# Kernel tuning notes

Hardware: AMD Instinct MI355X
Metric: run time of the kernel (lower is better)

Reference implementation:

```python
import jax, jax.numpy as jnp
import numpy as np

V, E, H, L = 512, 128, 256, 4
B, T = 128, 1024


def setup_inputs() -> dict:
    key = jax.random.key(0)
    ks = jax.random.split(key, 16)
    s = 0.05
    inp = {
        "x": jax.random.randint(ks[0], (B, T), 0, V),
        "tags": jax.random.randint(ks[1], (B, T), 0, L),
        "mask": jnp.ones((B, T), dtype=bool),
        "emb": jax.random.normal(ks[2], (V, E), jnp.float32) * s,
        "w_ih_f": jax.random.normal(ks[3], (3 * H, E), jnp.float32) * s,
        "w_hh_f": jax.random.normal(ks[4], (3 * H, H), jnp.float32) * s,
        "b_ih_f": jax.random.normal(ks[5], (3 * H,), jnp.float32) * s,
        "b_hh_f": jax.random.normal(ks[6], (3 * H,), jnp.float32) * s,
        "w_ih_b": jax.random.normal(ks[7], (3 * H, E), jnp.float32) * s,
        "w_hh_b": jax.random.normal(ks[8], (3 * H, H), jnp.float32) * s,
        "b_ih_b": jax.random.normal(ks[9], (3 * H,), jnp.float32) * s,
        "b_hh_b": jax.random.normal(ks[10], (3 * H,), jnp.float32) * s,
        "fc_w": jax.random.normal(ks[11], (L, 2 * H), jnp.float32) * s,
        "fc_b": jax.random.normal(ks[12], (L,), jnp.float32) * s,
        "start_trans": jax.random.normal(ks[13], (L,), jnp.float32) * 0.1,
        "end_trans": jax.random.normal(ks[14], (L,), jnp.float32) * 0.1,
        "trans": jax.random.normal(ks[15], (L, L), jnp.float32) * 0.1,
    }
    return inp


def _gru_scan(xe, w_ih, w_hh, b_ih, b_hh):
    # xe: [B,T,E] -> out [B,T,H]; PyTorch GRU gate order: r, z, n
    gi = jnp.einsum("bte,ge->btg", xe, w_ih) + b_ih  # [B,T,3H]
    gi = jnp.swapaxes(gi, 0, 1)  # [T,B,3H]
    h0 = jnp.zeros((xe.shape[0], H), xe.dtype)

    def step(h, gi_t):
        gh = h @ w_hh.T + b_hh
        i_r, i_z, i_n = jnp.split(gi_t, 3, axis=-1)
        h_r, h_z, h_n = jnp.split(gh, 3, axis=-1)
        r = jax.nn.sigmoid(i_r + h_r)
        z = jax.nn.sigmoid(i_z + h_z)
        n = jnp.tanh(i_n + r * h_n)
        h_new = (1.0 - z) * n + z * h
        return h_new, h_new

    _, out = jax.lax.scan(step, h0, gi)
    return jnp.swapaxes(out, 0, 1)  # [B,T,H]


def _crf_neg_llh(emissions, tags, mask, start_trans, end_trans, trans):
    # emissions [B,T,L], tags [B,T] int, mask [B,T] bool
    maskf = mask.astype(emissions.dtype)
    # ----- numerator: score of gold path -----
    em_sel = jnp.take_along_axis(emissions, tags[..., None], axis=2)[..., 0]  # [B,T]
    trans_sel = trans[tags[:, :-1], tags[:, 1:]]  # [B,T-1]
    score = start_trans[tags[:, 0]] + em_sel[:, 0]
    score = score + jnp.sum((trans_sel + em_sel[:, 1:]) * maskf[:, 1:], axis=1)
    seq_ends = jnp.sum(mask.astype(jnp.int32), axis=1) - 1  # [B]
    last_tags = jnp.take_along_axis(tags, seq_ends[:, None], axis=1)[:, 0]
    score = score + end_trans[last_tags]
    # ----- denominator: forward algorithm (logsumexp scan) -----
    alpha0 = start_trans[None, :] + emissions[:, 0]  # [B,L]
    em_rest = jnp.swapaxes(emissions[:, 1:], 0, 1)  # [T-1,B,L]
    m_rest = jnp.swapaxes(mask[:, 1:], 0, 1)  # [T-1,B]

    def step(alpha, inputs):
        emit_t, m_t = inputs
        nxt = jax.nn.logsumexp(alpha[:, :, None] + trans[None] + emit_t[:, None, :], axis=1)
        alpha = jnp.where(m_t[:, None], nxt, alpha)
        return alpha, None

    alpha, _ = jax.lax.scan(step, alpha0, (em_rest, m_rest))
    logZ = jax.nn.logsumexp(alpha + end_trans[None, :], axis=1)  # [B]
    llh = score - logZ
    return -jnp.mean(llh)  # reduction='mean', negated in Segmenter.forward


def reference(x, tags, mask, emb, w_ih_f, w_hh_f, b_ih_f, b_hh_f,
              w_ih_b, w_hh_b, b_ih_b, b_hh_b, fc_w, fc_b,
              start_trans, end_trans, trans):
    xe = emb[x]  # [B,T,E]
    out_f = _gru_scan(xe, w_ih_f, w_hh_f, b_ih_f, b_hh_f)
    out_b = _gru_scan(xe[:, ::-1], w_ih_b, w_hh_b, b_ih_b, b_hh_b)[:, ::-1]
    gru_out = jnp.concatenate([out_f, out_b], axis=-1)  # [B,T,2H]
    emissions = jnp.einsum("bth,lh->btl", gru_out, fc_w) + fc_b  # [B,T,L]
    return _crf_neg_llh(emissions, tags, mask, start_trans, end_trans, trans)
```

## Files before the change

### kernel.cpp

```cpp
#include <hip/hip_runtime.h>
#include <hip/hip_fp16.h>

#define Tn 1024
#define NB 128

#define S_RZ (-1.4426950408889634f)
#define S_N  (-2.8853900817779268f)

typedef _Float16 h2_t  __attribute__((ext_vector_type(2)));
typedef _Float16 f16x8 __attribute__((ext_vector_type(8)));
typedef float    f32x4 __attribute__((ext_vector_type(4)));

__device__ __forceinline__ float dot2f(h2_t a, h2_t b, float c) {
#if __has_builtin(__builtin_amdgcn_fdot2)
  return __builtin_amdgcn_fdot2(a, b, c, false);
#else
  return c + (float)a[0] * (float)b[0] + (float)a[1] * (float)b[1];
#endif
}

__device__ __forceinline__ h2_t u2h(unsigned u) {
  union { unsigned u; h2_t h; } c; c.u = u; return c.h;
}

template <int CTRL>
__device__ __forceinline__ float dppadd(float v) {
  int i = __builtin_bit_cast(int, v);
  int r = __builtin_amdgcn_update_dpp(i, i, CTRL, 0xF, 0xF, true);
  return v + __builtin_bit_cast(float, r);
}

__global__ __launch_bounds__(768)
void gv_build(const float* __restrict__ emb,
              const float* __restrict__ wihf, const float* __restrict__ bihf, const float* __restrict__ bhhf,
              const float* __restrict__ wihb, const float* __restrict__ bihb, const float* __restrict__ bhhb,
              float* __restrict__ gvp)
{
  const int d  = blockIdx.x >> 7;
  const int v4 = (blockIdx.x & 127) * 4;
  const float* wih = d ? wihb : wihf;
  const float* bih = d ? bihb : bihf;
  const float* bhh = d ? bhhb : bhhf;
  __shared__ float se[4][128];
  const int tid = threadIdx.x;
  if (tid < 512) se[tid >> 7][tid & 127] = emb[(v4 + (tid >> 7)) * 128 + (tid & 127)];
  __syncthreads();
  const int row = tid;
  const float b0 = bih[row];
  float a0 = b0, a1 = b0, a2 = b0, a3 = b0;
  #pragma unroll
  for (int e = 0; e < 128; e += 4) {
    const float4 w = *reinterpret_cast<const float4*>(&wih[row * 128 + e]);
    a0 = fmaf(w.x, se[0][e], a0); a0 = fmaf(w.y, se[0][e+1], a0);
    a0 = fmaf(w.z, se[0][e+2], a0); a0 = fmaf(w.w, se[0][e+3], a0);
    a1 = fmaf(w.x, se[1][e], a1); a1 = fmaf(w.y, se[1][e+1], a1);
    a1 = fmaf(w.z, se[1][e+2], a1); a1 = fmaf(w.w, se[1][e+3], a1);
    a2 = fmaf(w.x, se[2][e], a2); a2 = fmaf(w.y, se[2][e+1], a2);
    a2 = fmaf(w.z, se[2][e+2], a2); a2 = fmaf(w.w, se[2][e+3], a2);
    a3 = fmaf(w.x, se[3][e], a3); a3 = fmaf(w.y, se[3][e+1], a3);
    a3 = fmaf(w.z, se[3][e+2], a3); a3 = fmaf(w.w, se[3][e+3], a3);
  }
  const int g  = row >> 8, j = row & 255;
  const int w  = j >> 5, tu = (j >> 4) & 1, c = j & 15;
  const float sc  = (g == 2) ? S_N : S_RZ;
  const float add = (g < 2) ? bhh[row] : 0.f;
  const int slot = ((w * 2 + tu) * 3 + g) * 16 + c;
  float* out = gvp + (size_t)(d * 512 + v4) * 768 + slot;
  out[0]    = sc * (a0 + add);
  out[768]  = sc * (a1 + add);
  out[1536] = sc * (a2 + add);
  out[2304] = sc * (a3 + add);
}

__global__ __launch_bounds__(512, 2)
void gru_scan(const int* __restrict__ x,
              const float* __restrict__ gvp,
              const float* __restrict__ whhf,
              const float* __restrict__ whhb,
              const float* __restrict__ bhhf,
              const float* __restrict__ bhhb,
              const float* __restrict__ fcw,
              float* __restrict__ em)
{
  const int tid = threadIdx.x;
  const int w   = tid >> 6;
  const int l   = tid & 63;
  const int c   = l & 15;
  const int lg  = l >> 4;
  const int dir = blockIdx.x & 1;
  const int b   = blockIdx.x >> 1;

  const float* whh = dir ? whhb : whhf;
  const float* bhh = dir ? bhhb : bhhf;

  __shared__ __align__(16) _Float16 hls[2][256];
  __shared__ float gvs[2][768];
  __shared__ float els[2][8];

  if (tid < 64) reinterpret_cast<uint4*>(hls)[tid] = make_uint4(0, 0, 0, 0);

  f16x8 bf[3][2][8];
  #pragma unroll
  for (int g = 0; g < 3; ++g) {
    const float sc = (g == 2) ? S_N : S_RZ;
    #pragma unroll
    for (int tu = 0; tu < 2; ++tu) {
      const float* wrow = whh + (size_t)(g * 256 + w * 32 + tu * 16 + c) * 256 + lg * 8;
      #pragma unroll
      for (int ks = 0; ks < 8; ++ks) {
        const float4 f0 = *reinterpret_cast<const float4*>(wrow + ks * 32);
        const float4 f1 = *reinterpret_cast<const float4*>(wrow + ks * 32 + 4);
        f16x8 v;
        v[0] = (_Float16)(f0.x * sc); v[1] = (_Float16)(f0.y * sc);
        v[2] = (_Float16)(f0.z * sc); v[3] = (_Float16)(f0.w * sc);
        v[4] = (_Float16)(f1.x * sc); v[5] = (_Float16)(f1.y * sc);
        v[6] = (_Float16)(f1.z * sc); v[7] = (_Float16)(f1.w * sc);
        bf[g][tu][ks] = v;
      }
    }
  }

  const float bn0 = S_N * bhh[512 + w * 32 + c];
  const float bn1 = S_N * bhh[512 + w * 32 + 16 + c];

  const int lab = tid >> 7;
  const int kp  = tid & 127;
  h2_t fce;
  fce[0] = (_Float16)fcw[lab * 512 + dir * 256 + 2 * kp];
  fce[1] = (_Float16)fcw[lab * 512 + dir * 256 + 2 * kp + 1];

  const int*   xb  = x + b * Tn;
  float*       emo = em + (size_t)(dir * NB + b) * (Tn * 4);
  const float* gvd = gvp + (size_t)dir * (512 * 768);

  {
    const float* gr = gvd + (size_t)xb[dir ? (Tn - 1) : 0] * 768;
    gvs[0][tid] = gr[tid];
    if (tid < 256) gvs[0][tid + 512] = gr[tid + 512];
  }
  float ho0 = 0.f, ho1 = 0.f;
  __syncthreads();

  for (int t = 0; t < Tn; ++t) {
    const int cur = t & 1;

    const int tn1 = (t + 1 < Tn) ? (t + 1) : (Tn - 1);
    const float* gr = gvd + (size_t)xb[dir ? (Tn - 1 - tn1) : tn1] * 768;
    const float su0 = gr[tid];
    const float su1 = (tid < 256) ? gr[tid + 512] : 0.f;

    {
      const unsigned hq = *reinterpret_cast<const unsigned*>(&hls[cur][kp * 2]);
      float pa = dot2f(fce, u2h(hq), 0.f);
      pa = dppadd<0xB1>(pa);
      pa = dppadd<0x4E>(pa);
      pa = dppadd<0x141>(pa);
      pa = dppadd<0x140>(pa);
      pa += __shfl_xor(pa, 16);
      pa += __shfl_xor(pa, 32);
      if (l == 0) els[cur][w] = pa;
    }
    if (t >= 2 && tid < 4) {
      const float v = els[cur ^ 1][2 * tid] + els[cur ^ 1][2 * tid + 1];
      const int ptt = dir ? (Tn + 1 - t) : (t - 2);
      emo[ptt * 4 + tid] = v;
    }

    const float* gc = gvs[cur] + w * 96 + c;
    f32x4 aR0 = {gc[0],  0.f, 0.f, 0.f};
    f32x4 aZ0 = {gc[16], 0.f, 0.f, 0.f};
    f32x4 aN0 = {bn0,    0.f, 0.f, 0.f};
    f32x4 aR1 = {gc[48], 0.f, 0.f, 0.f};
    f32x4 aZ1 = {gc[64], 0.f, 0.f, 0.f};
    f32x4 aN1 = {bn1,    0.f, 0.f, 0.f};
    const float gin0 = gc[32];
    const float gin1 = gc[80];

    const _Float16* hc = hls[cur];
    #pragma unroll
    for (int ks = 0; ks < 4; ++ks) {
      const f16x8 a = *reinterpret_cast<const f16x8*>(hc + ks * 32 + lg * 8);
      aR0 = __builtin_amdgcn_mfma_f32_16x16x32_f16(a, bf[0][0][ks], aR0, 0, 0, 0);
      aZ0 = __builtin_amdgcn_mfma_f32_16x16x32_f16(a, bf[1][0][ks], aZ0, 0, 0, 0);
      aN0 = __builtin_amdgcn_mfma_f32_16x16x32_f16(a, bf[2][0][ks], aN0, 0, 0, 0);
      aR1 = __builtin_amdgcn_mfma_f32_16x16x32_f16(a, bf[0][1][ks], aR1, 0, 0, 0);
      aZ1 = __builtin_amdgcn_mfma_f32_16x16x32_f16(a, bf[1][1][ks], aZ1, 0, 0, 0);
      aN1 = __builtin_amdgcn_mfma_f32_16x16x32_f16(a, bf[2][1][ks], aN1, 0, 0, 0);
    }
    __builtin_amdgcn_sched_barrier(0);
    #pragma unroll
    for (int ks = 4; ks < 8; ++ks) {
      const f16x8 a = *reinterpret_cast<const f16x8*>(hc + ks * 32 + lg * 8);
      aR0 = __builtin_amdgcn_mfma_f32_16x16x32_f16(a, bf[0][0][ks], aR0, 0, 0, 0);
      aZ0 = __builtin_amdgcn_mfma_f32_16x16x32_f16(a, bf[1][0][ks], aZ0, 0, 0, 0);
      aN0 = __builtin_amdgcn_mfma_f32_16x16x32_f16(a, bf[2][0][ks], aN0, 0, 0, 0);
      aR1 = __builtin_amdgcn_mfma_f32_16x16x32_f16(a, bf[0][1][ks], aR1, 0, 0, 0);
      aZ1 = __builtin_amdgcn_mfma_f32_16x16x32_f16(a, bf[1][1][ks], aZ1, 0, 0, 0);
      aN1 = __builtin_amdgcn_mfma_f32_16x16x32_f16(a, bf[2][1][ks], aN1, 0, 0, 0);
    }

    {
      const float er0 = __builtin_amdgcn_exp2f(aR0[0]);
      const float rr0 = __builtin_amdgcn_rcpf(1.f + er0);
      const float ez0 = __builtin_amdgcn_exp2f(aZ0[0]);
      const float zz0 = __builtin_amdgcn_rcpf(1.f + ez0);
      float y0 = fmaf(rr0, aN0[0], gin0);
      y0 = fminf(y0, 126.f);
      const float en0 = __builtin_amdgcn_exp2f(y0);
      const float nn0 = (1.f - en0) * __builtin_amdgcn_rcpf(1.f + en0);
      const float h0 = fmaf(zz0, ho0 - nn0, nn0);

      const float er1 = __builtin_amdgcn_exp2f(aR1[0]);
      const float rr1 = __builtin_amdgcn_rcpf(1.f + er1);
      const float ez1 = __builtin_amdgcn_exp2f(aZ1[0]);
      const float zz1 = __builtin_amdgcn_rcpf(1.f + ez1);
      float y1 = fmaf(rr1, aN1[0], gin1);
      y1 = fminf(y1, 126.f);
      const float en1 = __builtin_amdgcn_exp2f(y1);
      const float nn1 = (1.f - en1) * __builtin_amdgcn_rcpf(1.f + en1);
      const float h1 = fmaf(zz1, ho1 - nn1, nn1);

      ho0 = h0; ho1 = h1;
      if (lg == 0) {
        hls[cur ^ 1][w * 32 + c]      = (_Float16)h0;
        hls[cur ^ 1][w * 32 + 16 + c] = (_Float16)h1;
      }
    }

    gvs[cur ^ 1][tid] = su0;
    if (tid < 256) gvs[cur ^ 1][tid + 512] = su1;
    __syncthreads();
  }

  if (tid < 4) {
    const float v = els[1][2 * tid] + els[1][2 * tid + 1];
    emo[(dir ? 1 : (Tn - 2)) * 4 + tid] = v;
  }
  {
    const unsigned hq = *reinterpret_cast<const unsigned*>(&hls[0][kp * 2]);
    float pa = dot2f(fce, u2h(hq), 0.f);
    pa = dppadd<0xB1>(pa);
    pa = dppadd<0x4E>(pa);
    pa = dppadd<0x141>(pa);
    pa = dppadd<0x140>(pa);
    pa += __shfl_xor(pa, 16);
    pa += __shfl_xor(pa, 32);
    if (l == 0) els[0][w] = pa;
  }
  __syncthreads();
  if (tid < 4) {
    const float v = els[0][2 * tid] + els[0][2 * tid + 1];
    emo[(dir ? 0 : (Tn - 1)) * 4 + tid] = v;
  }
}

__global__ __launch_bounds__(64)
void crf_nllh(const int* __restrict__ tags,
              const float* __restrict__ em,
              const float* __restrict__ fc_b,
              const float* __restrict__ st,
              const float* __restrict__ et,
              const float* __restrict__ tr,
              float* __restrict__ llh)
{
  const int lane = threadIdx.x;
  const int l = lane & 3;
  const int q = lane >> 2;
  const int b = blockIdx.x * 16 + q;
  const float* ef = em + (size_t)b * Tn * 4;
  const float* eb = em + ((size_t)NB + b) * Tn * 4;
  const int* tg = tags + b * Tn;
  const float fcb = fc_b[l];
  const float tc0 = tr[l * 4 + l];
  const float tc1 = tr[(l ^ 1) * 4 + l];
  const float tc2 = tr[(l ^ 2) * 4 + l];
  const float tc3 = tr[(l ^ 3) * 4 + l];

  const float e0 = ef[l] + eb[l] + fcb;
  float alpha = st[l] + e0;
  int tprev = tg[0];
  float score = (tprev == l) ? (st[l] + e0) : 0.f;

  #pragma unroll 8
  for (int t = 1; t < Tn; ++t) {
    const float e = ef[t * 4 + l] + eb[t * 4 + l] + fcb;
    const int tc = tg[t];
    if (tc == l) {
      const int s2 = tprev ^ l;
      const float tsel = (s2 & 1) ? ((s2 & 2) ? tc3 : tc1)
                                  : ((s2 & 2) ? tc2 : tc0);
      score += e + tsel;
    }
    tprev = tc;
    const float a1 = __shfl_xor(alpha, 1);
    const float a2 = __shfl_xor(alpha, 2);
    const float a3 = __shfl_xor(alpha, 3);
    const float v0 = alpha + tc0;
    const float v1 = a1 + tc1;
    const float v2 = a2 + tc2;
    const float v3 = a3 + tc3;
    const float mx = fmaxf(fmaxf(v0, v1), fmaxf(v2, v3));
    const float s = __expf(v0 - mx) + __expf(v1 - mx) + __expf(v2 - mx) + __expf(v3 - mx);
    alpha = mx + __logf(s) + e;
  }

  score += (tprev == l) ? et[l] : 0.f;
  float ae = alpha + et[l];
  float m1 = fmaxf(ae, __shfl_xor(ae, 1));
  m1 = fmaxf(m1, __shfl_xor(m1, 2));
  float se = __expf(ae - m1);
  se += __shfl_xor(se, 1);
  se += __shfl_xor(se, 2);
  const float logZ = m1 + __logf(se);
  float sc = score + __shfl_xor(score, 1);
  sc += __shfl_xor(sc, 2);
  if (l == 0) llh[b] = sc - logZ;
}

__global__ __launch_bounds__(128)
void reduce_mean(const float* __restrict__ llh, float* __restrict__ out)
{
  const int t = threadIdx.x;
  float v = llh[t];
  #pragma unroll
  for (int m = 32; m >= 1; m >>= 1) v += __shfl_xor(v, m);
  __shared__ float s2[2];
  if ((t & 63) == 0) s2[t >> 6] = v;
  __syncthreads();
  if (t == 0) out[0] = -(s2[0] + s2[1]) * (1.f / 128.f);
}

extern "C" void kernel_launch(void* const* d_in, const int* in_sizes, int n_in,
                              void* d_out, int out_size, void* d_ws, size_t ws_size,
                              hipStream_t stream) {
  const int*   x    = (const int*)d_in[0];
  const int*   tags = (const int*)d_in[1];
  const float* emb  = (const float*)d_in[3];
  const float* wihf = (const float*)d_in[4];
  const float* whhf = (const float*)d_in[5];
  const float* bihf = (const float*)d_in[6];
  const float* bhhf = (const float*)d_in[7];
  const float* wihb = (const float*)d_in[8];
  const float* whhb = (const float*)d_in[9];
  const float* bihb = (const float*)d_in[10];
  const float* bhhb = (const float*)d_in[11];
  const float* fcw  = (const float*)d_in[12];
  const float* fcb  = (const float*)d_in[13];
  const float* st   = (const float*)d_in[14];
  const float* et   = (const float*)d_in[15];
  const float* tr   = (const float*)d_in[16];

  char* ws = (char*)d_ws;
  float* gvp = (float*)ws;
  float* em  = (float*)(ws + 3145728);
  float* llh = (float*)(ws + 3145728 + 4194304);

  gv_build<<<dim3(256), dim3(768), 0, stream>>>(emb, wihf, bihf, bhhf, wihb, bihb, bhhb, gvp);
  gru_scan<<<dim3(256), dim3(512), 0, stream>>>(x, gvp, whhf, whhb, bhhf, bhhb, fcw, em);
  crf_nllh<<<dim3(8), dim3(64), 0, stream>>>(tags, em, fcb, st, et, tr, llh);
  reduce_mean<<<dim3(1), dim3(128), 0, stream>>>(llh, (float*)d_out);
}
```

Before: 1.759 ms.

## Halve GRU scan block to 4 waves with 64 hidden units per wave

The recurrent GRU kernel now runs 256 threads (4 waves) per sequence instead of 512, with each wave owning 64 hidden units and holding twice as many recurrent weight fragments in AGPRs via inline-asm MFMAs. The input-gate table layout is reinterleaved so each lane reads its 12 gate preactivations with three vector LDS loads. The per-step emission dot product is now done per wave per label with direct global stores, replacing the shared-memory staging and the extra reduction step. Token indices are prefetched two steps ahead. The aim is to shrink barrier cost and per-step latency in the serial scan, at the cost of higher register pressure, lower occupancy and a hand-placed s_nop hazard wait.

```diff
diff --git a/kernel.cpp b/kernel.cpp
--- a/kernel.cpp
+++ b/kernel.cpp
@@ -21,13 +21,6 @@
 
 __device__ __forceinline__ h2_t u2h(unsigned u) {
   union { unsigned u; h2_t h; } c; c.u = u; return c.h;
-}
-
-template <int CTRL>
-__device__ __forceinline__ float dppadd(float v) {
-  int i = __builtin_bit_cast(int, v);
-  int r = __builtin_amdgcn_update_dpp(i, i, CTRL, 0xF, 0xF, true);
-  return v + __builtin_bit_cast(float, r);
 }
 
 __global__ __launch_bounds__(768)
@@ -61,10 +54,10 @@
     a3 = fmaf(w.z, se[3][e+2], a3); a3 = fmaf(w.w, se[3][e+3], a3);
   }
   const int g  = row >> 8, j = row & 255;
-  const int w  = j >> 5, tu = (j >> 4) & 1, c = j & 15;
+  const int w  = j >> 6, tb = (j >> 4) & 3, c = j & 15;
   const float sc  = (g == 2) ? S_N : S_RZ;
   const float add = (g < 2) ? bhh[row] : 0.f;
-  const int slot = ((w * 2 + tu) * 3 + g) * 16 + c;
+  const int slot = w * 192 + c * 12 + tb * 3 + g;
   float* out = gvp + (size_t)(d * 512 + v4) * 768 + slot;
   out[0]    = sc * (a0 + add);
   out[768]  = sc * (a1 + add);
@@ -72,7 +65,33 @@
   out[2304] = sc * (a3 + add);
 }
 
-__global__ __launch_bounds__(512, 2)
+#define MFMA_Z(D, A, B) \
+  asm("v_mfma_f32_16x16x32_f16 %0, %1, %2, %3" : "=&v"(D) : "v"(A), "a"(B), "v"(ZQv))
+#define MFMA_A(D, A, B) \
+  asm("v_mfma_f32_16x16x32_f16 %0, %1, %2, %0" : "+v"(D) : "v"(A), "a"(B))
+
+#define ROW12(MAC, AF, ks) \
+  MAC(aR0, AF, bf[0][0][ks]); MAC(aZ0, AF, bf[1][0][ks]); MAC(aN0, AF, bf[2][0][ks]); \
+  MAC(aR1, AF, bf[0][1][ks]); MAC(aZ1, AF, bf[1][1][ks]); MAC(aN1, AF, bf[2][1][ks]); \
+  MAC(aR2, AF, bf[0][2][ks]); MAC(aZ2, AF, bf[1][2][ks]); MAC(aN2, AF, bf[2][2][ks]); \
+  MAC(aR3, AF, bf[0][3][ks]); MAC(aZ3, AF, bf[1][3][ks]); MAC(aN3, AF, bf[2][3][ks]);
+
+#define UPD(tb, AR, AZ, AN) { \
+  const float pr = gvv[3*(tb)+0] + AR[0]; \
+  const float er = __builtin_amdgcn_exp2f(pr); \
+  const float rr = __builtin_amdgcn_rcpf(1.f + er); \
+  const float pz = gvv[3*(tb)+1] + AZ[0]; \
+  const float ez = __builtin_amdgcn_exp2f(pz); \
+  const float zz = __builtin_amdgcn_rcpf(1.f + ez); \
+  float y = fmaf(rr, AN[0] + bn[tb], gvv[3*(tb)+2]); \
+  y = fminf(y, 126.f); \
+  const float en = __builtin_amdgcn_exp2f(y); \
+  const float nn = (1.f - en) * __builtin_amdgcn_rcpf(1.f + en); \
+  const float hnew = fmaf(zz, ho##tb - nn, nn); \
+  ho##tb = hnew; \
+  if (lg == 0) hls[cur ^ 1][w * 64 + (tb) * 16 + c] = (_Float16)hnew; }
+
+__global__ __launch_bounds__(256, 1)
 void gru_scan(const int* __restrict__ x,
               const float* __restrict__ gvp,
               const float* __restrict__ whhf,
@@ -95,17 +114,16 @@
 
   __shared__ __align__(16) _Float16 hls[2][256];
   __shared__ float gvs[2][768];
-  __shared__ float els[2][8];
 
   if (tid < 64) reinterpret_cast<uint4*>(hls)[tid] = make_uint4(0, 0, 0, 0);
 
-  f16x8 bf[3][2][8];
+  f16x8 bf[3][4][8];
   #pragma unroll
   for (int g = 0; g < 3; ++g) {
     const float sc = (g == 2) ? S_N : S_RZ;
     #pragma unroll
-    for (int tu = 0; tu < 2; ++tu) {
-      const float* wrow = whh + (size_t)(g * 256 + w * 32 + tu * 16 + c) * 256 + lg * 8;
+    for (int tb = 0; tb < 4; ++tb) {
+      const float* wrow = whh + (size_t)(g * 256 + w * 64 + tb * 16 + c) * 256 + lg * 8;
       #pragma unroll
       for (int ks = 0; ks < 8; ++ks) {
         const float4 f0 = *reinterpret_cast<const float4*>(wrow + ks * 32);
@@ -115,142 +133,106 @@
         v[2] = (_Float16)(f0.z * sc); v[3] = (_Float16)(f0.w * sc);
         v[4] = (_Float16)(f1.x * sc); v[5] = (_Float16)(f1.y * sc);
         v[6] = (_Float16)(f1.z * sc); v[7] = (_Float16)(f1.w * sc);
-        bf[g][tu][ks] = v;
+        bf[g][tb][ks] = v;
       }
     }
   }
 
-  const float bn0 = S_N * bhh[512 + w * 32 + c];
-  const float bn1 = S_N * bhh[512 + w * 32 + 16 + c];
-
-  const int lab = tid >> 7;
-  const int kp  = tid & 127;
-  h2_t fce;
-  fce[0] = (_Float16)fcw[lab * 512 + dir * 256 + 2 * kp];
-  fce[1] = (_Float16)fcw[lab * 512 + dir * 256 + 2 * kp + 1];
+  float bn[4];
+  #pragma unroll
+  for (int tb = 0; tb < 4; ++tb) bn[tb] = S_N * bhh[512 + w * 64 + tb * 16 + c];
+
+  h2_t fce0, fce1;
+  fce0[0] = (_Float16)fcw[w * 512 + dir * 256 + 2 * l];
+  fce0[1] = (_Float16)fcw[w * 512 + dir * 256 + 2 * l + 1];
+  fce1[0] = (_Float16)fcw[w * 512 + dir * 256 + 128 + 2 * l];
+  fce1[1] = (_Float16)fcw[w * 512 + dir * 256 + 128 + 2 * l + 1];
+
+  f32x4 ZQv = {0.f, 0.f, 0.f, 0.f};
 
   const int*   xb  = x + b * Tn;
   float*       emo = em + (size_t)(dir * NB + b) * (Tn * 4);
   const float* gvd = gvp + (size_t)dir * (512 * 768);
 
+  int tok1;
   {
-    const float* gr = gvd + (size_t)xb[dir ? (Tn - 1) : 0] * 768;
-    gvs[0][tid] = gr[tid];
-    if (tid < 256) gvs[0][tid + 512] = gr[tid + 512];
-  }
-  float ho0 = 0.f, ho1 = 0.f;
+    const int tk0 = xb[dir ? (Tn - 1) : 0];
+    const float* g0 = gvd + (size_t)tk0 * 768;
+    gvs[0][tid]       = g0[tid];
+    gvs[0][tid + 256] = g0[tid + 256];
+    gvs[0][tid + 512] = g0[tid + 512];
+    tok1 = xb[dir ? (Tn - 2) : 1];
+  }
+  float ho0 = 0.f, ho1 = 0.f, ho2 = 0.f, ho3 = 0.f;
   __syncthreads();
 
   for (int t = 0; t < Tn; ++t) {
     const int cur = t & 1;
 
-    const int tn1 = (t + 1 < Tn) ? (t + 1) : (Tn - 1);
-    const float* gr = gvd + (size_t)xb[dir ? (Tn - 1 - tn1) : tn1] * 768;
+    const float* gr = gvd + (size_t)tok1 * 768;
     const float su0 = gr[tid];
-    const float su1 = (tid < 256) ? gr[tid + 512] : 0.f;
-
+    const float su1 = gr[tid + 256];
+    const float su2 = gr[tid + 512];
     {
-      const unsigned hq = *reinterpret_cast<const unsigned*>(&hls[cur][kp * 2]);
-      float pa = dot2f(fce, u2h(hq), 0.f);
-      pa = dppadd<0xB1>(pa);
-      pa = dppadd<0x4E>(pa);
-      pa = dppadd<0x141>(pa);
-      pa = dppadd<0x140>(pa);
-      pa += __shfl_xor(pa, 16);
-      pa += __shfl_xor(pa, 32);
-      if (l == 0) els[cur][w] = pa;
-    }
-    if (t >= 2 && tid < 4) {
-      const float v = els[cur ^ 1][2 * tid] + els[cur ^ 1][2 * tid + 1];
-      const int ptt = dir ? (Tn + 1 - t) : (t - 2);
-      emo[ptt * 4 + tid] = v;
-    }
-
-    const float* gc = gvs[cur] + w * 96 + c;
-    f32x4 aR0 = {gc[0],  0.f, 0.f, 0.f};
-    f32x4 aZ0 = {gc[16], 0.f, 0.f, 0.f};
-    f32x4 aN0 = {bn0,    0.f, 0.f, 0.f};
-    f32x4 aR1 = {gc[48], 0.f, 0.f, 0.f};
-    f32x4 aZ1 = {gc[64], 0.f, 0.f, 0.f};
-    f32x4 aN1 = {bn1,    0.f, 0.f, 0.f};
-    const float gin0 = gc[32];
-    const float gin1 = gc[80];
-
-    const _Float16* hc = hls[cur];
-    #pragma unroll
-    for (int ks = 0; ks < 4; ++ks) {
-      const f16x8 a = *reinterpret_cast<const f16x8*>(hc + ks * 32 + lg * 8);
-      aR0 = __builtin_amdgcn_mfma_f32_16x16x32_f16(a, bf[0][0][ks], aR0, 0, 0, 0);
-      aZ0 = __builtin_amdgcn_mfma_f32_16x16x32_f16(a, bf[1][0][ks], aZ0, 0, 0, 0);
-      aN0 = __builtin_amdgcn_mfma_f32_16x16x32_f16(a, bf[2][0][ks], aN0, 0, 0, 0);
-      aR1 = __builtin_amdgcn_mfma_f32_16x16x32_f16(a, bf[0][1][ks], aR1, 0, 0, 0);
-      aZ1 = __builtin_amdgcn_mfma_f32_16x16x32_f16(a, bf[1][1][ks], aZ1, 0, 0, 0);
-      aN1 = __builtin_amdgcn_mfma_f32_16x16x32_f16(a, bf[2][1][ks], aN1, 0, 0, 0);
-    }
+      const int s2 = (t + 2 < Tn) ? (t + 2) : (Tn - 1);
+      tok1 = xb[dir ? (Tn - 1 - s2) : s2];
+    }
+
+    if (t > 0) {
+      const unsigned hw0 = *reinterpret_cast<const unsigned*>(&hls[cur][2 * l]);
+      const unsigned hw1 = *reinterpret_cast<const unsigned*>(&hls[cur][2 * l + 128]);
+      float pa = dot2f(fce0, u2h(hw0), 0.f);
+      pa = dot2f(fce1, u2h(hw1), pa);
+      pa += __shfl_xor(pa, 1);  pa += __shfl_xor(pa, 2);  pa += __shfl_xor(pa, 4);
+      pa += __shfl_xor(pa, 8);  pa += __shfl_xor(pa, 16); pa += __shfl_xor(pa, 32);
+      if (l == 0) emo[(size_t)(dir ? (Tn - t) : (t - 1)) * 4 + w] = pa;
+    }
+
+    const f32x4* gq = reinterpret_cast<const f32x4*>(gvs[cur] + w * 192 + c * 12);
+    const f32x4 q0 = gq[0], q1 = gq[1], q2 = gq[2];
+    float gvv[12];
+    gvv[0] = q0[0]; gvv[1]  = q0[1]; gvv[2]  = q0[2]; gvv[3]  = q0[3];
+    gvv[4] = q1[0]; gvv[5]  = q1[1]; gvv[6]  = q1[2]; gvv[7]  = q1[3];
+    gvv[8] = q2[0]; gvv[9]  = q2[1]; gvv[10] = q2[2]; gvv[11] = q2[3];
+
+    const f16x8* hap = reinterpret_cast<const f16x8*>(&hls[cur][lg * 8]);
+    f32x4 aR0, aZ0, aN0, aR1, aZ1, aN1, aR2, aZ2, aN2, aR3, aZ3, aN3;
+    {
+      const f16x8 af0 = hap[0], af1 = hap[4], af2 = hap[8], af3 = hap[12];
+      ROW12(MFMA_Z, af0, 0)
+      ROW12(MFMA_A, af1, 1)
+      ROW12(MFMA_A, af2, 2)
+      ROW12(MFMA_A, af3, 3)
+    }
+    {
+      const f16x8 af4 = hap[16], af5 = hap[20], af6 = hap[24], af7 = hap[28];
+      ROW12(MFMA_A, af4, 4)
+      ROW12(MFMA_A, af5, 5)
+      ROW12(MFMA_A, af6, 6)
+      ROW12(MFMA_A, af7, 7)
+    }
+    asm volatile("s_nop 7\n\ts_nop 3");
     __builtin_amdgcn_sched_barrier(0);
-    #pragma unroll
-    for (int ks = 4; ks < 8; ++ks) {
-      const f16x8 a = *reinterpret_cast<const f16x8*>(hc + ks * 32 + lg * 8);
-      aR0 = __builtin_amdgcn_mfma_f32_16x16x32_f16(a, bf[0][0][ks], aR0, 0, 0, 0);
-      aZ0 = __builtin_amdgcn_mfma_f32_16x16x32_f16(a, bf[1][0][ks], aZ0, 0, 0, 0);
-      aN0 = __builtin_amdgcn_mfma_f32_16x16x32_f16(a, bf[2][0][ks], aN0, 0, 0, 0);
-      aR1 = __builtin_amdgcn_mfma_f32_16x16x32_f16(a, bf[0][1][ks], aR1, 0, 0, 0);
-      aZ1 = __builtin_amdgcn_mfma_f32_16x16x32_f16(a, bf[1][1][ks], aZ1, 0, 0, 0);
-      aN1 = __builtin_amdgcn_mfma_f32_16x16x32_f16(a, bf[2][1][ks], aN1, 0, 0, 0);
-    }
-
-    {
-      const float er0 = __builtin_amdgcn_exp2f(aR0[0]);
-      const float rr0 = __builtin_amdgcn_rcpf(1.f + er0);
-      const float ez0 = __builtin_amdgcn_exp2f(aZ0[0]);
-      const float zz0 = __builtin_amdgcn_rcpf(1.f + ez0);
-      float y0 = fmaf(rr0, aN0[0], gin0);
-      y0 = fminf(y0, 126.f);
-      const float en0 = __builtin_amdgcn_exp2f(y0);
-      const float nn0 = (1.f - en0) * __builtin_amdgcn_rcpf(1.f + en0);
-      const float h0 = fmaf(zz0, ho0 - nn0, nn0);
-
-      const float er1 = __builtin_amdgcn_exp2f(aR1[0]);
-      const float rr1 = __builtin_amdgcn_rcpf(1.f + er1);
-      const float ez1 = __builtin_amdgcn_exp2f(aZ1[0]);
-      const float zz1 = __builtin_amdgcn_rcpf(1.f + ez1);
-      float y1 = fmaf(rr1, aN1[0], gin1);
-      y1 = fminf(y1, 126.f);
-      const float en1 = __builtin_amdgcn_exp2f(y1);
-      const float nn1 = (1.f - en1) * __builtin_amdgcn_rcpf(1.f + en1);
-      const float h1 = fmaf(zz1, ho1 - nn1, nn1);
-
-      ho0 = h0; ho1 = h1;
-      if (lg == 0) {
-        hls[cur ^ 1][w * 32 + c]      = (_Float16)h0;
-        hls[cur ^ 1][w * 32 + 16 + c] = (_Float16)h1;
-      }
-    }
-
-    gvs[cur ^ 1][tid] = su0;
-    if (tid < 256) gvs[cur ^ 1][tid + 512] = su1;
+
+    UPD(0, aR0, aZ0, aN0)
+    UPD(1, aR1, aZ1, aN1)
+    UPD(2, aR2, aZ2, aN2)
+    UPD(3, aR3, aZ3, aN3)
+
+    gvs[cur ^ 1][tid]       = su0;
+    gvs[cur ^ 1][tid + 256] = su1;
+    gvs[cur ^ 1][tid + 512] = su2;
     __syncthreads();
   }
 
-  if (tid < 4) {
-    const float v = els[1][2 * tid] + els[1][2 * tid + 1];
-    emo[(dir ? 1 : (Tn - 2)) * 4 + tid] = v;
-  }
   {
-    const unsigned hq = *reinterpret_cast<const unsigned*>(&hls[0][kp * 2]);
-    float pa = dot2f(fce, u2h(hq), 0.f);
-    pa = dppadd<0xB1>(pa);
-    pa = dppadd<0x4E>(pa);
-    pa = dppadd<0x141>(pa);
-    pa = dppadd<0x140>(pa);
-    pa += __shfl_xor(pa, 16);
-    pa += __shfl_xor(pa, 32);
-    if (l == 0) els[0][w] = pa;
-  }
-  __syncthreads();
-  if (tid < 4) {
-    const float v = els[0][2 * tid] + els[0][2 * tid + 1];
-    emo[(dir ? 0 : (Tn - 1)) * 4 + tid] = v;
+    const unsigned hw0 = *reinterpret_cast<const unsigned*>(&hls[0][2 * l]);
+    const unsigned hw1 = *reinterpret_cast<const unsigned*>(&hls[0][2 * l + 128]);
+    float pa = dot2f(fce0, u2h(hw0), 0.f);
+    pa = dot2f(fce1, u2h(hw1), pa);
+    pa += __shfl_xor(pa, 1);  pa += __shfl_xor(pa, 2);  pa += __shfl_xor(pa, 4);
+    pa += __shfl_xor(pa, 8);  pa += __shfl_xor(pa, 16); pa += __shfl_xor(pa, 32);
+    if (l == 0) emo[(size_t)(dir ? 0 : (Tn - 1)) * 4 + w] = pa;
   }
 }
 
@@ -356,7 +338,7 @@
   float* llh = (float*)(ws + 3145728 + 4194304);
 
   gv_build<<<dim3(256), dim3(768), 0, stream>>>(emb, wihf, bihf, bhhf, wihb, bihb, bhhb, gvp);
-  gru_scan<<<dim3(256), dim3(512), 0, stream>>>(x, gvp, whhf, whhb, bhhf, bhhb, fcw, em);
+  gru_scan<<<dim3(256), dim3(256), 0, stream>>>(x, gvp, whhf, whhb, bhhf, bhhb, fcw, em);
   crf_nllh<<<dim3(8), dim3(64), 0, stream>>>(tags, em, fcb, st, et, tr, llh);
   reduce_mean<<<dim3(1), dim3(128), 0, stream>>>(llh, (float*)d_out);
 }
```

Result: slower. 2.275 ms (+29.3%).
